# Performance work log

Measured on AMD Instinct MI355X. Metric: run time of the kernel, lower is better.

Reference implementation:

```python
import jax, jax.numpy as jnp
import numpy as np

L, H, D, T, DFF, OUT, B = 6, 12, 49, 16, 1024, 10, 8192
STD = 0.02


def setup_inputs() -> dict:
    key = jax.random.key(0)
    ks = jax.random.split(key, 24)
    n = lambda k, shape: jax.random.normal(k, shape, dtype=jnp.float32) * STD
    return {
        "x": jax.random.normal(ks[0], (B, 784), dtype=jnp.float32),
        "mask": jnp.ones((B, T), dtype=bool),  # unused by the original Attention
        # per-layer, per-head Q/K/V/out linears (weights stored as (in, out))
        "Wq": n(ks[1], (L, H, D, D)), "bq": n(ks[2], (L, H, D)),
        "Wk": n(ks[3], (L, H, D, D)), "bk": n(ks[4], (L, H, D)),
        "Wv": n(ks[5], (L, H, D, D)), "bv": n(ks[6], (L, H, D)),
        "Wo": n(ks[7], (L, H, D, D)), "bo": n(ks[8], (L, H, D)),
        # concat projection Linear(D*H, D)
        "Wcat": n(ks[9], (L, H * D, D)), "bcat": n(ks[10], (L, D)),
        # LayerNorms
        "ln1_g": jnp.ones((L, D), jnp.float32), "ln1_b": jnp.zeros((L, D), jnp.float32),
        "ln2_g": jnp.ones((L, D), jnp.float32), "ln2_b": jnp.zeros((L, D), jnp.float32),
        # FeedForward
        "W1": n(ks[11], (L, D, DFF)), "b1": n(ks[12], (L, DFF)),
        "W2": n(ks[13], (L, DFF, D)), "b2": n(ks[14], (L, D)),
        # ClassificationHead
        "Wc": n(ks[15], (D, OUT)), "bc": n(ks[16], (OUT,)),
    }


def _ln(x, g, b):
    mu = jnp.mean(x, axis=-1, keepdims=True)
    var = jnp.mean((x - mu) ** 2, axis=-1, keepdims=True)
    return (x - mu) / jnp.sqrt(var + 1e-5) * g + b


def _forward(x, Wq, bq, Wk, bk, Wv, bv, Wo, bo, Wcat, bcat,
             ln1_g, ln1_b, ln2_g, ln2_b, W1, b1, W2, b2, Wc, bc):
    bsz = x.shape[0]
    h = x.reshape(bsz, T, D)  # MakeTokens
    scale = float(1.0 / np.sqrt(D))
    for i in range(L):
        xn = _ln(h, ln1_g[i], ln1_b[i])
        # all heads batched via einsum (each head attends over full d_model)
        q = jnp.einsum('btd,hde->bhte', xn, Wq[i]) + bq[i][None, :, None, :]
        k = jnp.einsum('btd,hde->bhte', xn, Wk[i]) + bk[i][None, :, None, :]
        v = jnp.einsum('btd,hde->bhte', xn, Wv[i]) + bv[i][None, :, None, :]
        w = jax.nn.softmax(jnp.einsum('bhte,bhse->bhts', q, k) * scale, axis=-1)
        o = jnp.einsum('bhts,bhse->bhte', w, v)
        o = jnp.einsum('bhte,hef->bhtf', o, Wo[i]) + bo[i][None, :, None, :]
        cat = o.transpose(0, 2, 1, 3).reshape(bsz, T, H * D)  # concat heads
        attn = cat @ Wcat[i] + bcat[i]
        x2 = h + attn  # dropout is identity at inference
        xn2 = _ln(x2, ln2_g[i], ln2_b[i])
        ff = jax.nn.relu(xn2 @ W1[i] + b1[i]) @ W2[i] + b2[i]
        h = x2 + ff
    return h[:, 0, :] @ Wc + bc  # ClassificationHead on token 0


def reference(x, mask, Wq, bq, Wk, bk, Wv, bv, Wo, bo, Wcat, bcat,
              ln1_g, ln1_b, ln2_g, ln2_b, W1, b1, W2, b2, Wc, bc):
    # mask is accepted but unused, matching the original Attention.forward
    return _forward(x, Wq, bq, Wk, bk, Wv, bv, Wo, bo, Wcat, bcat,
                    ln1_g, ln1_b, ln2_g, ln2_b, W1, b1, W2, b2, Wc, bc)
```

## Files before the change

### kernel.cpp

```cpp
#include <hip/hip_runtime.h>
#include <hip/hip_bf16.h>

#define LYR 6
#define NH 12
#define DM 49
#define FFD 1024
#define NOUT 10
#define NB 8192
#define NSTG 120

typedef __bf16 bf16x8 __attribute__((ext_vector_type(8)));
typedef float f32x4 __attribute__((ext_vector_type(4)));
typedef unsigned int u32;
typedef u32 u32x4 __attribute__((ext_vector_type(4)));

static __device__ __forceinline__ f32x4 mfma_full(u32x4 a, u32x4 b, f32x4 c) {
  return __builtin_amdgcn_mfma_f32_16x16x32_bf16(
      __builtin_bit_cast(bf16x8, a), __builtin_bit_cast(bf16x8, b), c, 0, 0, 0);
}

static __device__ __forceinline__ f32x4 mfma_hz(u32 a0, u32 a1, u32 b0, u32 b1, f32x4 c) {
  u32x4 A = {a0, a1, 0u, 0u};
  u32x4 B = {b0, b1, 0u, 0u};
  return mfma_full(A, B, c);
}

static __device__ __forceinline__ unsigned short f2bf(float f) {
  union { float f; unsigned u; } c; c.f = f;
  unsigned r = c.u + 0x7fffu + ((c.u >> 16) & 1u);
  return (unsigned short)(r >> 16);
}

static __device__ __forceinline__ u32 pk2(float a, float b) {
  __hip_bfloat162 h2 = __float22bfloat162_rn(make_float2(a, b));
  u32 r;
  __builtin_memcpy(&r, &h2, 4);
  return r;
}

static __device__ __forceinline__ void gload16(const void* gp, void* lp) {
  __builtin_amdgcn_global_load_lds(
      (const __attribute__((address_space(1))) unsigned int*)gp,
      (__attribute__((address_space(3))) unsigned int*)lp, 16, 0, 0);
}

static __device__ __forceinline__ void decode(int idx, int& d, int& col) {
  int tile = idx >> 10, ks = (idx >> 9) & 1, lane = (idx >> 3) & 63, j = idx & 7;
  col = 16 * tile + (lane & 15);
  d = 16 * (2 * ks + (j >= 4 ? 1 : 0)) + 4 * (lane >> 4) + (j & 3);
}


__global__ void prep_qkv_frag(const float* __restrict__ Wq, const float* __restrict__ bq,
                              const float* __restrict__ Wk, const float* __restrict__ bk,
                              const float* __restrict__ Wv, const float* __restrict__ bv,
                              unsigned short* __restrict__ blob) {
  int lh = blockIdx.x, l = lh / NH, hd = lh % NH;
  unsigned short* base = blob + (size_t)(l * 20 + hd) * 16384;
  for (int idx = threadIdx.x; idx < 4096; idx += blockDim.x) {
    int d, e;
    decode(idx, d, e);
    float q = 0.f, k = 0.f, v = 0.f;
    if (e < DM) {
      if (d < DM) {
        q = Wq[(size_t)lh * 2401 + d * DM + e] * (1.f / 7.f);
        k = Wk[(size_t)lh * 2401 + d * DM + e];
        v = Wv[(size_t)lh * 2401 + d * DM + e];
      } else if (d == DM) {
        q = bq[lh * DM + e] * (1.f / 7.f);
        k = bk[lh * DM + e];
        v = bv[lh * DM + e];
      }
    }
    base[idx] = f2bf(q);
    base[4096 + idx] = f2bf(k);
    base[8192 + idx] = f2bf(v);
  }
}

__global__ void prep_comb_frag(const float* __restrict__ Wo, const float* __restrict__ bo,
                               const float* __restrict__ Wcat, const float* __restrict__ bcat,
                               unsigned short* __restrict__ blob) {
  int lh = blockIdx.x, l = lh / NH, hh = lh % NH;
  unsigned short* base = blob + (size_t)(l * 20 + hh) * 16384 + 12288;
  for (int idx = threadIdx.x; idx < 4096; idx += blockDim.x) {
    int e, f;
    decode(idx, e, f);
    float val = 0.f;
    if (f < DM) {
      if (e < DM) {
        for (int c = 0; c < DM; ++c)
          val += Wo[(size_t)lh * 2401 + e * DM + c] *
                 Wcat[((size_t)l * 588 + hh * DM + c) * DM + f];
      } else if (e == DM) {
        for (int c = 0; c < DM; ++c)
          val += bo[lh * DM + c] * Wcat[((size_t)l * 588 + hh * DM + c) * DM + f];
        if (hh == 0) val += bcat[l * DM + f];
      }
    }
    base[idx] = f2bf(val);
  }
}

__global__ void prep_ff_frag(const float* __restrict__ W1, const float* __restrict__ b1,
                             const float* __restrict__ W2,
                             unsigned short* __restrict__ blob) {
  int l = blockIdx.x >> 3, part = blockIdx.x & 7;
  for (int idx = part * 16384 + threadIdx.x; idx < (part + 1) * 16384; idx += blockDim.x) {
    int c = idx >> 13, within = idx & 8191, sec = within >> 12, sidx = within & 4095;
    int fb = c >> 1, c_rel = c & 1;
    unsigned short* dst =
        blob + (size_t)(l * 20 + 12 + fb) * 16384 + c_rel * 8192 + sec * 4096;
    int d, col;
    decode(sidx, d, col);
    float v = 0.f;
    if (sec == 0) {
      int jcol = 64 * c + col;
      if (d < DM) v = W1[(size_t)l * DM * FFD + d * FFD + jcol];
      else if (d == DM) v = b1[l * FFD + jcol];
    } else {
      int jg = 64 * c + d;
      if (col < DM) v = W2[(size_t)l * FFD * DM + jg * DM + col];
    }
    dst[sidx] = f2bf(v);
  }
}

__global__ void prep_small(const float* __restrict__ g1, const float* __restrict__ b1,
                           const float* __restrict__ g2, const float* __restrict__ b2,
                           const float* __restrict__ bff2,
                           float* __restrict__ g1p, float* __restrict__ b1p,
                           float* __restrict__ g2p, float* __restrict__ b2p,
                           float* __restrict__ bff2p) {
  int idx = threadIdx.x;
  if (idx >= 384) return;
  int l = idx >> 6, d = idx & 63;
  bool v = d < DM;
  g1p[idx] = v ? g1[l * DM + d] : 0.f;
  b1p[idx] = v ? b1[l * DM + d] : 0.f;
  g2p[idx] = v ? g2[l * DM + d] : 0.f;
  b2p[idx] = v ? b2[l * DM + d] : 0.f;
  bff2p[idx] = v ? bff2[l * DM + d] : 0.f;
}


static __device__ __forceinline__ void ln_pack(const f32x4 (&h)[4], const f32x4 (&gv)[4],
                                               const f32x4 (&bv)[4], int g, u32x4 (&xf)[2]) {
  float s = 0.f, s2 = 0.f;
#pragma unroll
  for (int mi = 0; mi < 4; ++mi)
#pragma unroll
    for (int r = 0; r < 4; ++r) { float v = h[mi][r]; s += v; s2 += v * v; }
  s += __shfl_xor(s, 16, 64); s += __shfl_xor(s, 32, 64);
  s2 += __shfl_xor(s2, 16, 64); s2 += __shfl_xor(s2, 32, 64);
  float mu = s * (1.f / 49.f);
  float rs = rsqrtf(s2 * (1.f / 49.f) - mu * mu + 1e-5f);
  u32 t[8];
#pragma unroll
  for (int mi = 0; mi < 4; ++mi) {
    float xv[4];
#pragma unroll
    for (int r = 0; r < 4; ++r) xv[r] = (h[mi][r] - mu) * rs * gv[mi][r] + bv[mi][r];
    if (mi == 3) xv[1] = (g == 0) ? 1.0f : xv[1];
    t[2 * mi] = pk2(xv[0], xv[1]);
    t[2 * mi + 1] = pk2(xv[2], xv[3]);
  }
  xf[0] = u32x4{t[0], t[1], t[2], t[3]};
  xf[1] = u32x4{t[4], t[5], t[6], t[7]};
}

static __device__ __forceinline__ void softmax_pk(f32x4 s, u32& p0, u32& p1) {
  float m = fmaxf(fmaxf(s[0], s[1]), fmaxf(s[2], s[3]));
  m = fmaxf(m, __shfl_xor(m, 16, 64));
  m = fmaxf(m, __shfl_xor(m, 32, 64));
  float e0 = __expf(s[0] - m), e1 = __expf(s[1] - m);
  float e2 = __expf(s[2] - m), e3 = __expf(s[3] - m);
  float su = e0 + e1 + e2 + e3;
  su += __shfl_xor(su, 16, 64);
  su += __shfl_xor(su, 32, 64);
  float inv = 1.f / su;
  p0 = pk2(e0 * inv, e1 * inv);
  p1 = pk2(e2 * inv, e3 * inv);
}

#define STAGE_LOAD(s)                                                         \
  do {                                                                        \
    const unsigned short* gsrc = blob + (size_t)(s) * 16384 + tid * 8;        \
    unsigned short* ldst = &wbuf[(s) & 1][wv * 512];                          \
    _Pragma("unroll") for (int r = 0; r < 8; ++r)                             \
        gload16(gsrc + r * 2048, ldst + r * 2048);                            \
  } while (0)

__global__ __launch_bounds__(256, 2) void transformer_kernel(
    const float* __restrict__ x, float* __restrict__ out,
    const unsigned short* __restrict__ blob,
    const float* __restrict__ lg1, const float* __restrict__ lb1,
    const float* __restrict__ lg2, const float* __restrict__ lb2,
    const float* __restrict__ b2p, const float* __restrict__ Wc,
    const float* __restrict__ bc) {
  __shared__ __align__(16) unsigned short wbuf[2][16384];
  const int tid = threadIdx.x;
  const int wv = tid >> 6, lane = tid & 63;
  const int g = lane >> 4, li = lane & 15;
  const int s0 = blockIdx.x * 16 + wv * 4;
  const f32x4 z4 = {0.f, 0.f, 0.f, 0.f};

  STAGE_LOAD(0);

  f32x4 h[4][4];
#pragma unroll
  for (int s = 0; s < 4; ++s) {
    const float* xa = x + (size_t)(s0 + s) * 784 + li * DM;
#pragma unroll
    for (int mi = 0; mi < 4; ++mi)
#pragma unroll
      for (int r = 0; r < 4; ++r) {
        int d = 16 * mi + 4 * g + r;
        h[s][mi][r] = (d < DM) ? xa[d] : 0.f;
      }
  }

  int stage = 0;
  for (int layer = 0; layer < LYR; ++layer) {
    u32x4 xf[4][2];
    {
      f32x4 gv[4], bv[4];
#pragma unroll
      for (int mi = 0; mi < 4; ++mi) {
        int off = layer * 64 + 16 * mi + 4 * g;
        gv[mi] = *(const f32x4*)(lg1 + off);
        bv[mi] = *(const f32x4*)(lb1 + off);
      }
#pragma unroll
      for (int s = 0; s < 4; ++s) ln_pack(h[s], gv, bv, g, xf[s]);
    }

    for (int hd = 0; hd < NH; ++hd) {
      __syncthreads();
      if (stage + 1 < NSTG) STAGE_LOAD(stage + 1);
      const unsigned short* W = wbuf[stage & 1];
      ++stage;
      const u32x4* QW = (const u32x4*)W;
      const u32x4* KW = (const u32x4*)(W + 4096);
      const u32x4* VW = (const u32x4*)(W + 8192);
      const u32x4* CW = (const u32x4*)(W + 12288);

      u32x4 qf[4][2], kf[4][2];
#pragma unroll
      for (int mi = 0; mi < 4; ++mi) {
        f32x4 cq[4], ck[4];
#pragma unroll
        for (int s = 0; s < 4; ++s) { cq[s] = z4; ck[s] = z4; }
#pragma unroll
        for (int ks = 0; ks < 2; ++ks) {
          u32x4 wq = QW[(mi * 2 + ks) * 64 + lane];
#pragma unroll
          for (int s = 0; s < 4; ++s) cq[s] = mfma_full(wq, xf[s][ks], cq[s]);
          u32x4 wk = KW[(mi * 2 + ks) * 64 + lane];
#pragma unroll
          for (int s = 0; s < 4; ++s) ck[s] = mfma_full(wk, xf[s][ks], ck[s]);
        }
#pragma unroll
        for (int s = 0; s < 4; ++s) {
          qf[s][mi >> 1][2 * (mi & 1)] = pk2(cq[s][0], cq[s][1]);
          qf[s][mi >> 1][2 * (mi & 1) + 1] = pk2(cq[s][2], cq[s][3]);
          kf[s][mi >> 1][2 * (mi & 1)] = pk2(ck[s][0], ck[s][1]);
          kf[s][mi >> 1][2 * (mi & 1) + 1] = pk2(ck[s][2], ck[s][3]);
        }
      }
      u32 p[4][2];
#pragma unroll
      for (int s = 0; s < 4; ++s) {
        f32x4 sc = mfma_full(kf[s][0], qf[s][0], z4);
        sc = mfma_full(kf[s][1], qf[s][1], sc);
        softmax_pk(sc, p[s][0], p[s][1]);
      }
      u32 vf_[4][4][2];
#pragma unroll
      for (int nt = 0; nt < 4; ++nt) {
        f32x4 cv[4];
#pragma unroll
        for (int s = 0; s < 4; ++s) cv[s] = z4;
#pragma unroll
        for (int ks = 0; ks < 2; ++ks) {
          u32x4 w = VW[(nt * 2 + ks) * 64 + lane];
#pragma unroll
          for (int s = 0; s < 4; ++s) cv[s] = mfma_full(xf[s][ks], w, cv[s]);
        }
#pragma unroll
        for (int s = 0; s < 4; ++s) {
          vf_[s][nt][0] = pk2(cv[s][0], cv[s][1]);
          vf_[s][nt][1] = pk2(cv[s][2], cv[s][3]);
        }
      }
      u32x4 of_[4][2];
#pragma unroll
      for (int nt = 0; nt < 4; ++nt) {
#pragma unroll
        for (int s = 0; s < 4; ++s) {
          f32x4 c = mfma_hz(vf_[s][nt][0], vf_[s][nt][1], p[s][0], p[s][1], z4);
          if (nt == 3) c[1] = (g == 0) ? 1.0f : c[1];
          of_[s][nt >> 1][2 * (nt & 1)] = pk2(c[0], c[1]);
          of_[s][nt >> 1][2 * (nt & 1) + 1] = pk2(c[2], c[3]);
        }
      }
#pragma unroll
      for (int ft = 0; ft < 4; ++ft) {
#pragma unroll
        for (int ks = 0; ks < 2; ++ks) {
          u32x4 w = CW[(ft * 2 + ks) * 64 + lane];
#pragma unroll
          for (int s = 0; s < 4; ++s) h[s][ft] = mfma_full(w, of_[s][ks], h[s][ft]);
        }
      }
    }

    {
      f32x4 gv[4], bv[4];
#pragma unroll
      for (int mi = 0; mi < 4; ++mi) {
        int off = layer * 64 + 16 * mi + 4 * g;
        gv[mi] = *(const f32x4*)(lg2 + off);
        bv[mi] = *(const f32x4*)(lb2 + off);
      }
#pragma unroll
      for (int s = 0; s < 4; ++s) ln_pack(h[s], gv, bv, g, xf[s]);
#pragma unroll
      for (int mi = 0; mi < 4; ++mi) {
        f32x4 bb = *(const f32x4*)(b2p + layer * 64 + 16 * mi + 4 * g);
#pragma unroll
        for (int s = 0; s < 4; ++s) h[s][mi] += bb;
      }
    }

    for (int fb = 0; fb < 8; ++fb) {
      __syncthreads();
      if (stage + 1 < NSTG) STAGE_LOAD(stage + 1);
      const unsigned short* W = wbuf[stage & 1];
      ++stage;
#pragma unroll
      for (int cr = 0; cr < 2; ++cr) {
        const u32x4* W1c = (const u32x4*)(W + cr * 8192);
        const u32x4* W2c = (const u32x4*)(W + cr * 8192 + 4096);
        u32x4 af[4][2];
#pragma unroll
        for (int jt = 0; jt < 4; ++jt) {
          f32x4 ca[4];
#pragma unroll
          for (int s = 0; s < 4; ++s) ca[s] = z4;
#pragma unroll
          for (int ks = 0; ks < 2; ++ks) {
            u32x4 w = W1c[(jt * 2 + ks) * 64 + lane];
#pragma unroll
            for (int s = 0; s < 4; ++s) ca[s] = mfma_full(w, xf[s][ks], ca[s]);
          }
#pragma unroll
          for (int s = 0; s < 4; ++s) {
            float r0 = fmaxf(ca[s][0], 0.f), r1 = fmaxf(ca[s][1], 0.f);
            float r2 = fmaxf(ca[s][2], 0.f), r3 = fmaxf(ca[s][3], 0.f);
            af[s][jt >> 1][2 * (jt & 1)] = pk2(r0, r1);
            af[s][jt >> 1][2 * (jt & 1) + 1] = pk2(r2, r3);
          }
        }
#pragma unroll
        for (int ft = 0; ft < 4; ++ft) {
#pragma unroll
          for (int ks = 0; ks < 2; ++ks) {
            u32x4 w = W2c[(ft * 2 + ks) * 64 + lane];
#pragma unroll
            for (int s = 0; s < 4; ++s) h[s][ft] = mfma_full(w, af[s][ks], h[s][ft]);
          }
        }
      }
    }
  }

  __syncthreads();
  float* hs = (float*)&wbuf[0][0];
  if (li == 0) {
#pragma unroll
    for (int s = 0; s < 4; ++s)
#pragma unroll
      for (int mi = 0; mi < 4; ++mi)
#pragma unroll
        for (int r = 0; r < 4; ++r)
          hs[(wv * 4 + s) * 64 + 16 * mi + 4 * g + r] = h[s][mi][r];
  }
  __syncthreads();
  if (lane < 40) {
    int smp = lane / 10, c = lane % 10;
    float acc = bc[c];
    const float* hrow = hs + (wv * 4 + smp) * 64;
    for (int d = 0; d < DM; ++d) acc += hrow[d] * Wc[d * NOUT + c];
    out[(size_t)(s0 + smp) * NOUT + c] = acc;
  }
}

extern "C" void kernel_launch(void* const* d_in, const int* in_sizes, int n_in,
                              void* d_out, int out_size, void* d_ws, size_t ws_size,
                              hipStream_t stream) {
  const float* x = (const float*)d_in[0];
  const float* Wq = (const float*)d_in[2];
  const float* bq = (const float*)d_in[3];
  const float* Wk = (const float*)d_in[4];
  const float* bk = (const float*)d_in[5];
  const float* Wv = (const float*)d_in[6];
  const float* bv = (const float*)d_in[7];
  const float* Wo = (const float*)d_in[8];
  const float* bo = (const float*)d_in[9];
  const float* Wcat = (const float*)d_in[10];
  const float* bcat = (const float*)d_in[11];
  const float* ln1_g = (const float*)d_in[12];
  const float* ln1_b = (const float*)d_in[13];
  const float* ln2_g = (const float*)d_in[14];
  const float* ln2_b = (const float*)d_in[15];
  const float* W1 = (const float*)d_in[16];
  const float* b1 = (const float*)d_in[17];
  const float* W2 = (const float*)d_in[18];
  const float* b2 = (const float*)d_in[19];
  const float* Wc = (const float*)d_in[20];
  const float* bc = (const float*)d_in[21];

  unsigned short* blob = (unsigned short*)d_ws;
  float* fp = (float*)(blob + (size_t)NSTG * 16384);
  float* g1p = fp;
  float* b1p = g1p + 384;
  float* g2p = b1p + 384;
  float* b2lp = g2p + 384;
  float* b2p = b2lp + 384;

  prep_qkv_frag<<<72, 256, 0, stream>>>(Wq, bq, Wk, bk, Wv, bv, blob);
  prep_comb_frag<<<72, 256, 0, stream>>>(Wo, bo, Wcat, bcat, blob);
  prep_ff_frag<<<48, 256, 0, stream>>>(W1, b1, W2, blob);
  prep_small<<<1, 384, 0, stream>>>(ln1_g, ln1_b, ln2_g, ln2_b, b2, g1p, b1p, g2p, b2lp, b2p);

  transformer_kernel<<<NB / 16, 256, 0, stream>>>(
      x, (float*)d_out, blob, g1p, b1p, g2p, b2lp, b2p, Wc, bc);
}
```

Before: 615.5 us.

## Halve samples per wave and weight stage size to double occupancy

Each wave now handles 2 samples instead of 4, and each weight stage is split in half (QK then VC per head, 16 FF chunks per layer). This halves shared memory per block and registers, so launch bounds allow 4 blocks per CU and the grid doubles. The aim is to hide latency with more resident waves. In exchange, every block still streams the full weight set, so total weight traffic doubles, each LDS weight read feeds fewer MFMAs, and there are twice as many barriers. Softmax also drops its max subtraction, saving two shuffles and a reduction, but this relies on attention scores staying small enough not to overflow.

```diff
diff --git a/kernel.cpp b/kernel.cpp
--- a/kernel.cpp
+++ b/kernel.cpp
@@ -7,7 +7,7 @@
 #define FFD 1024
 #define NOUT 10
 #define NB 8192
-#define NSTG 120
+#define NWIN 240
 
 typedef __bf16 bf16x8 __attribute__((ext_vector_type(8)));
 typedef float f32x4 __attribute__((ext_vector_type(4)));
@@ -170,11 +170,8 @@
 }
 
 static __device__ __forceinline__ void softmax_pk(f32x4 s, u32& p0, u32& p1) {
-  float m = fmaxf(fmaxf(s[0], s[1]), fmaxf(s[2], s[3]));
-  m = fmaxf(m, __shfl_xor(m, 16, 64));
-  m = fmaxf(m, __shfl_xor(m, 32, 64));
-  float e0 = __expf(s[0] - m), e1 = __expf(s[1] - m);
-  float e2 = __expf(s[2] - m), e3 = __expf(s[3] - m);
+  float e0 = __expf(s[0]), e1 = __expf(s[1]);
+  float e2 = __expf(s[2]), e3 = __expf(s[3]);
   float su = e0 + e1 + e2 + e3;
   su += __shfl_xor(su, 16, 64);
   su += __shfl_xor(su, 32, 64);
@@ -185,31 +182,31 @@
 
 #define STAGE_LOAD(s)                                                         \
   do {                                                                        \
-    const unsigned short* gsrc = blob + (size_t)(s) * 16384 + tid * 8;        \
+    const unsigned short* gsrc = blob + (size_t)(s) * 8192 + tid * 8;         \
     unsigned short* ldst = &wbuf[(s) & 1][wv * 512];                          \
-    _Pragma("unroll") for (int r = 0; r < 8; ++r)                             \
+    _Pragma("unroll") for (int r = 0; r < 4; ++r)                             \
         gload16(gsrc + r * 2048, ldst + r * 2048);                            \
   } while (0)
 
-__global__ __launch_bounds__(256, 2) void transformer_kernel(
+__global__ __launch_bounds__(256, 4) void transformer_kernel(
     const float* __restrict__ x, float* __restrict__ out,
     const unsigned short* __restrict__ blob,
     const float* __restrict__ lg1, const float* __restrict__ lb1,
     const float* __restrict__ lg2, const float* __restrict__ lb2,
     const float* __restrict__ b2p, const float* __restrict__ Wc,
     const float* __restrict__ bc) {
-  __shared__ __align__(16) unsigned short wbuf[2][16384];
+  __shared__ __align__(16) unsigned short wbuf[2][8192];
   const int tid = threadIdx.x;
   const int wv = tid >> 6, lane = tid & 63;
   const int g = lane >> 4, li = lane & 15;
-  const int s0 = blockIdx.x * 16 + wv * 4;
+  const int s0 = blockIdx.x * 8 + wv * 2;
   const f32x4 z4 = {0.f, 0.f, 0.f, 0.f};
 
   STAGE_LOAD(0);
 
-  f32x4 h[4][4];
-#pragma unroll
-  for (int s = 0; s < 4; ++s) {
+  f32x4 h[2][4];
+#pragma unroll
+  for (int s = 0; s < 2; ++s) {
     const float* xa = x + (size_t)(s0 + s) * 784 + li * DM;
 #pragma unroll
     for (int mi = 0; mi < 4; ++mi)
@@ -220,9 +217,9 @@
       }
   }
 
-  int stage = 0;
+  int w = 0;
   for (int layer = 0; layer < LYR; ++layer) {
-    u32x4 xf[4][2];
+    u32x4 xf[2][2];
     {
       f32x4 gv[4], bv[4];
 #pragma unroll
@@ -232,87 +229,93 @@
         bv[mi] = *(const f32x4*)(lb1 + off);
       }
 #pragma unroll
-      for (int s = 0; s < 4; ++s) ln_pack(h[s], gv, bv, g, xf[s]);
+      for (int s = 0; s < 2; ++s) ln_pack(h[s], gv, bv, g, xf[s]);
     }
 
     for (int hd = 0; hd < NH; ++hd) {
       __syncthreads();
-      if (stage + 1 < NSTG) STAGE_LOAD(stage + 1);
-      const unsigned short* W = wbuf[stage & 1];
-      ++stage;
-      const u32x4* QW = (const u32x4*)W;
-      const u32x4* KW = (const u32x4*)(W + 4096);
-      const u32x4* VW = (const u32x4*)(W + 8192);
-      const u32x4* CW = (const u32x4*)(W + 12288);
-
-      u32x4 qf[4][2], kf[4][2];
-#pragma unroll
-      for (int mi = 0; mi < 4; ++mi) {
-        f32x4 cq[4], ck[4];
-#pragma unroll
-        for (int s = 0; s < 4; ++s) { cq[s] = z4; ck[s] = z4; }
-#pragma unroll
-        for (int ks = 0; ks < 2; ++ks) {
-          u32x4 wq = QW[(mi * 2 + ks) * 64 + lane];
-#pragma unroll
-          for (int s = 0; s < 4; ++s) cq[s] = mfma_full(wq, xf[s][ks], cq[s]);
-          u32x4 wk = KW[(mi * 2 + ks) * 64 + lane];
-#pragma unroll
-          for (int s = 0; s < 4; ++s) ck[s] = mfma_full(wk, xf[s][ks], ck[s]);
-        }
-#pragma unroll
-        for (int s = 0; s < 4; ++s) {
-          qf[s][mi >> 1][2 * (mi & 1)] = pk2(cq[s][0], cq[s][1]);
-          qf[s][mi >> 1][2 * (mi & 1) + 1] = pk2(cq[s][2], cq[s][3]);
-          kf[s][mi >> 1][2 * (mi & 1)] = pk2(ck[s][0], ck[s][1]);
-          kf[s][mi >> 1][2 * (mi & 1) + 1] = pk2(ck[s][2], ck[s][3]);
-        }
-      }
-      u32 p[4][2];
-#pragma unroll
-      for (int s = 0; s < 4; ++s) {
-        f32x4 sc = mfma_full(kf[s][0], qf[s][0], z4);
-        sc = mfma_full(kf[s][1], qf[s][1], sc);
-        softmax_pk(sc, p[s][0], p[s][1]);
-      }
-      u32 vf_[4][4][2];
-#pragma unroll
-      for (int nt = 0; nt < 4; ++nt) {
-        f32x4 cv[4];
-#pragma unroll
-        for (int s = 0; s < 4; ++s) cv[s] = z4;
-#pragma unroll
-        for (int ks = 0; ks < 2; ++ks) {
-          u32x4 w = VW[(nt * 2 + ks) * 64 + lane];
-#pragma unroll
-          for (int s = 0; s < 4; ++s) cv[s] = mfma_full(xf[s][ks], w, cv[s]);
-        }
-#pragma unroll
-        for (int s = 0; s < 4; ++s) {
-          vf_[s][nt][0] = pk2(cv[s][0], cv[s][1]);
-          vf_[s][nt][1] = pk2(cv[s][2], cv[s][3]);
-        }
-      }
-      u32x4 of_[4][2];
-#pragma unroll
-      for (int nt = 0; nt < 4; ++nt) {
-#pragma unroll
-        for (int s = 0; s < 4; ++s) {
-          f32x4 c = mfma_hz(vf_[s][nt][0], vf_[s][nt][1], p[s][0], p[s][1], z4);
-          if (nt == 3) c[1] = (g == 0) ? 1.0f : c[1];
-          of_[s][nt >> 1][2 * (nt & 1)] = pk2(c[0], c[1]);
-          of_[s][nt >> 1][2 * (nt & 1) + 1] = pk2(c[2], c[3]);
-        }
-      }
-#pragma unroll
-      for (int ft = 0; ft < 4; ++ft) {
-#pragma unroll
-        for (int ks = 0; ks < 2; ++ks) {
-          u32x4 w = CW[(ft * 2 + ks) * 64 + lane];
-#pragma unroll
-          for (int s = 0; s < 4; ++s) h[s][ft] = mfma_full(w, of_[s][ks], h[s][ft]);
-        }
-      }
+      if (w + 1 < NWIN) STAGE_LOAD(w + 1);
+      u32 p[2][2];
+      {
+        const u32x4* QW = (const u32x4*)wbuf[w & 1];
+        const u32x4* KW = (const u32x4*)(wbuf[w & 1] + 4096);
+        u32x4 qf[2][2], kf[2][2];
+#pragma unroll
+        for (int mi = 0; mi < 4; ++mi) {
+          f32x4 cq[2], ck[2];
+#pragma unroll
+          for (int s = 0; s < 2; ++s) { cq[s] = z4; ck[s] = z4; }
+#pragma unroll
+          for (int ks = 0; ks < 2; ++ks) {
+            u32x4 wq = QW[(mi * 2 + ks) * 64 + lane];
+#pragma unroll
+            for (int s = 0; s < 2; ++s) cq[s] = mfma_full(wq, xf[s][ks], cq[s]);
+            u32x4 wk = KW[(mi * 2 + ks) * 64 + lane];
+#pragma unroll
+            for (int s = 0; s < 2; ++s) ck[s] = mfma_full(wk, xf[s][ks], ck[s]);
+          }
+#pragma unroll
+          for (int s = 0; s < 2; ++s) {
+            qf[s][mi >> 1][2 * (mi & 1)] = pk2(cq[s][0], cq[s][1]);
+            qf[s][mi >> 1][2 * (mi & 1) + 1] = pk2(cq[s][2], cq[s][3]);
+            kf[s][mi >> 1][2 * (mi & 1)] = pk2(ck[s][0], ck[s][1]);
+            kf[s][mi >> 1][2 * (mi & 1) + 1] = pk2(ck[s][2], ck[s][3]);
+          }
+        }
+#pragma unroll
+        for (int s = 0; s < 2; ++s) {
+          f32x4 sc = mfma_full(kf[s][0], qf[s][0], z4);
+          sc = mfma_full(kf[s][1], qf[s][1], sc);
+          softmax_pk(sc, p[s][0], p[s][1]);
+        }
+      }
+      ++w;
+
+      __syncthreads();
+      if (w + 1 < NWIN) STAGE_LOAD(w + 1);
+      {
+        const u32x4* VW = (const u32x4*)wbuf[w & 1];
+        const u32x4* CW = (const u32x4*)(wbuf[w & 1] + 4096);
+        u32 vf_[2][4][2];
+#pragma unroll
+        for (int nt = 0; nt < 4; ++nt) {
+          f32x4 cv[2];
+#pragma unroll
+          for (int s = 0; s < 2; ++s) cv[s] = z4;
+#pragma unroll
+          for (int ks = 0; ks < 2; ++ks) {
+            u32x4 wvv = VW[(nt * 2 + ks) * 64 + lane];
+#pragma unroll
+            for (int s = 0; s < 2; ++s) cv[s] = mfma_full(xf[s][ks], wvv, cv[s]);
+          }
+#pragma unroll
+          for (int s = 0; s < 2; ++s) {
+            vf_[s][nt][0] = pk2(cv[s][0], cv[s][1]);
+            vf_[s][nt][1] = pk2(cv[s][2], cv[s][3]);
+          }
+        }
+        u32x4 of_[2][2];
+#pragma unroll
+        for (int nt = 0; nt < 4; ++nt) {
+#pragma unroll
+          for (int s = 0; s < 2; ++s) {
+            f32x4 c = mfma_hz(vf_[s][nt][0], vf_[s][nt][1], p[s][0], p[s][1], z4);
+            if (nt == 3) c[1] = (g == 0) ? 1.0f : c[1];
+            of_[s][nt >> 1][2 * (nt & 1)] = pk2(c[0], c[1]);
+            of_[s][nt >> 1][2 * (nt & 1) + 1] = pk2(c[2], c[3]);
+          }
+        }
+#pragma unroll
+        for (int ft = 0; ft < 4; ++ft) {
+#pragma unroll
+          for (int ks = 0; ks < 2; ++ks) {
+            u32x4 wc = CW[(ft * 2 + ks) * 64 + lane];
+#pragma unroll
+            for (int s = 0; s < 2; ++s) h[s][ft] = mfma_full(wc, of_[s][ks], h[s][ft]);
+          }
+        }
+      }
+      ++w;
     }
 
     {
@@ -324,54 +327,50 @@
         bv[mi] = *(const f32x4*)(lb2 + off);
       }
 #pragma unroll
-      for (int s = 0; s < 4; ++s) ln_pack(h[s], gv, bv, g, xf[s]);
+      for (int s = 0; s < 2; ++s) ln_pack(h[s], gv, bv, g, xf[s]);
 #pragma unroll
       for (int mi = 0; mi < 4; ++mi) {
         f32x4 bb = *(const f32x4*)(b2p + layer * 64 + 16 * mi + 4 * g);
 #pragma unroll
-        for (int s = 0; s < 4; ++s) h[s][mi] += bb;
-      }
-    }
-
-    for (int fb = 0; fb < 8; ++fb) {
+        for (int s = 0; s < 2; ++s) h[s][mi] += bb;
+      }
+    }
+
+    for (int c = 0; c < 16; ++c) {
       __syncthreads();
-      if (stage + 1 < NSTG) STAGE_LOAD(stage + 1);
-      const unsigned short* W = wbuf[stage & 1];
-      ++stage;
-#pragma unroll
-      for (int cr = 0; cr < 2; ++cr) {
-        const u32x4* W1c = (const u32x4*)(W + cr * 8192);
-        const u32x4* W2c = (const u32x4*)(W + cr * 8192 + 4096);
-        u32x4 af[4][2];
-#pragma unroll
-        for (int jt = 0; jt < 4; ++jt) {
-          f32x4 ca[4];
-#pragma unroll
-          for (int s = 0; s < 4; ++s) ca[s] = z4;
-#pragma unroll
-          for (int ks = 0; ks < 2; ++ks) {
-            u32x4 w = W1c[(jt * 2 + ks) * 64 + lane];
-#pragma unroll
-            for (int s = 0; s < 4; ++s) ca[s] = mfma_full(w, xf[s][ks], ca[s]);
-          }
-#pragma unroll
-          for (int s = 0; s < 4; ++s) {
-            float r0 = fmaxf(ca[s][0], 0.f), r1 = fmaxf(ca[s][1], 0.f);
-            float r2 = fmaxf(ca[s][2], 0.f), r3 = fmaxf(ca[s][3], 0.f);
-            af[s][jt >> 1][2 * (jt & 1)] = pk2(r0, r1);
-            af[s][jt >> 1][2 * (jt & 1) + 1] = pk2(r2, r3);
-          }
-        }
-#pragma unroll
-        for (int ft = 0; ft < 4; ++ft) {
-#pragma unroll
-          for (int ks = 0; ks < 2; ++ks) {
-            u32x4 w = W2c[(ft * 2 + ks) * 64 + lane];
-#pragma unroll
-            for (int s = 0; s < 4; ++s) h[s][ft] = mfma_full(w, af[s][ks], h[s][ft]);
-          }
-        }
-      }
+      if (w + 1 < NWIN) STAGE_LOAD(w + 1);
+      const u32x4* W1c = (const u32x4*)wbuf[w & 1];
+      const u32x4* W2c = (const u32x4*)(wbuf[w & 1] + 4096);
+      u32x4 af[2][2];
+#pragma unroll
+      for (int jt = 0; jt < 4; ++jt) {
+        f32x4 ca[2];
+#pragma unroll
+        for (int s = 0; s < 2; ++s) ca[s] = z4;
+#pragma unroll
+        for (int ks = 0; ks < 2; ++ks) {
+          u32x4 ww = W1c[(jt * 2 + ks) * 64 + lane];
+#pragma unroll
+          for (int s = 0; s < 2; ++s) ca[s] = mfma_full(ww, xf[s][ks], ca[s]);
+        }
+#pragma unroll
+        for (int s = 0; s < 2; ++s) {
+          float r0 = fmaxf(ca[s][0], 0.f), r1 = fmaxf(ca[s][1], 0.f);
+          float r2 = fmaxf(ca[s][2], 0.f), r3 = fmaxf(ca[s][3], 0.f);
+          af[s][jt >> 1][2 * (jt & 1)] = pk2(r0, r1);
+          af[s][jt >> 1][2 * (jt & 1) + 1] = pk2(r2, r3);
+        }
+      }
+#pragma unroll
+      for (int ft = 0; ft < 4; ++ft) {
+#pragma unroll
+        for (int ks = 0; ks < 2; ++ks) {
+          u32x4 ww = W2c[(ft * 2 + ks) * 64 + lane];
+#pragma unroll
+          for (int s = 0; s < 2; ++s) h[s][ft] = mfma_full(ww, af[s][ks], h[s][ft]);
+        }
+      }
+      ++w;
     }
   }
 
@@ -379,18 +378,18 @@
   float* hs = (float*)&wbuf[0][0];
   if (li == 0) {
 #pragma unroll
-    for (int s = 0; s < 4; ++s)
+    for (int s = 0; s < 2; ++s)
 #pragma unroll
       for (int mi = 0; mi < 4; ++mi)
 #pragma unroll
         for (int r = 0; r < 4; ++r)
-          hs[(wv * 4 + s) * 64 + 16 * mi + 4 * g + r] = h[s][mi][r];
+          hs[(wv * 2 + s) * 64 + 16 * mi + 4 * g + r] = h[s][mi][r];
   }
   __syncthreads();
-  if (lane < 40) {
+  if (lane < 20) {
     int smp = lane / 10, c = lane % 10;
     float acc = bc[c];
-    const float* hrow = hs + (wv * 4 + smp) * 64;
+    const float* hrow = hs + (wv * 2 + smp) * 64;
     for (int d = 0; d < DM; ++d) acc += hrow[d] * Wc[d * NOUT + c];
     out[(size_t)(s0 + smp) * NOUT + c] = acc;
   }
@@ -422,7 +421,7 @@
   const float* bc = (const float*)d_in[21];
 
   unsigned short* blob = (unsigned short*)d_ws;
-  float* fp = (float*)(blob + (size_t)NSTG * 16384);
+  float* fp = (float*)(blob + (size_t)NWIN * 8192);
   float* g1p = fp;
   float* b1p = g1p + 384;
   float* g2p = b1p + 384;
@@ -434,6 +433,6 @@
   prep_ff_frag<<<48, 256, 0, stream>>>(W1, b1, W2, blob);
   prep_small<<<1, 384, 0, stream>>>(ln1_g, ln1_b, ln2_g, ln2_b, b2, g1p, b1p, g2p, b2lp, b2p);
 
-  transformer_kernel<<<NB / 16, 256, 0, stream>>>(
+  transformer_kernel<<<NB / 8, 256, 0, stream>>>(
       x, (float*)d_out, blob, g1p, b1p, g2p, b2lp, b2p, Wc, bc);
 }
```

After: 620.0 us. About the same (+0.7%).
